# Kernel optimization log

Measured on AMD Instinct MI355X. Metric: run time of the kernel, lower is better.

## Reference

```python
import jax, jax.numpy as jnp
import numpy as np

B, S, D, H = 4, 2048, 1024, 16
DK = D // H
DFF = 4 * D
EPS = 1e-6


def setup_inputs() -> dict:
    key = jax.random.key(0)
    ks = jax.random.split(key, 16)
    s = 0.02
    return {
        "x": jax.random.normal(ks[0], (B, S, D), jnp.float32),
        "mask": jax.random.randint(ks[1], (B, 1, 1, S), 0, 2, jnp.int32),
        "wq": jax.random.normal(ks[2], (D, D), jnp.float32) * s,
        "bq": jnp.zeros((D,), jnp.float32),
        "wk": jax.random.normal(ks[3], (D, D), jnp.float32) * s,
        "bk": jnp.zeros((D,), jnp.float32),
        "wv": jax.random.normal(ks[4], (D, D), jnp.float32) * s,
        "bv": jnp.zeros((D,), jnp.float32),
        "wo": jax.random.normal(ks[5], (D, D), jnp.float32) * s,
        "bo": jnp.zeros((D,), jnp.float32),
        "w1": jax.random.normal(ks[6], (DFF, D), jnp.float32) * s,
        "b1": jnp.zeros((DFF,), jnp.float32),
        "w2": jax.random.normal(ks[7], (D, DFF), jnp.float32) * s,
        "b2": jnp.zeros((D,), jnp.float32),
        "a1": jnp.ones((1,), jnp.float32),
        "c1": jnp.zeros((1,), jnp.float32),
        "a2": jnp.ones((1,), jnp.float32),
        "c2": jnp.zeros((1,), jnp.float32),
    }


def _layernorm(x, alpha, bias):
    # source: alpha * (x - mean) / (std + eps) + bias, torch std is unbiased
    mean = jnp.mean(x, axis=-1, keepdims=True)
    std = jnp.std(x, axis=-1, keepdims=True, ddof=1)
    return alpha * (x - mean) / (std + EPS) + bias


def _mha(x, mask, wq, bq, wk, bk, wv, bv, wo, bo):
    q = (x @ wq.T + bq).reshape(B, S, H, DK).transpose(0, 2, 1, 3)  # [B,H,S,DK]
    k = (x @ wk.T + bk).reshape(B, S, H, DK).transpose(0, 2, 1, 3)
    v = (x @ wv.T + bv).reshape(B, S, H, DK).transpose(0, 2, 1, 3)
    scores = jnp.einsum("bhqd,bhkd->bhqk", q, k) / jnp.sqrt(jnp.float32(DK))
    scores = jnp.where(mask == 0, jnp.float32(-1e9), scores)
    attn = jax.nn.softmax(scores, axis=-1)
    out = jnp.einsum("bhqk,bhkd->bhqd", attn, v)  # [B,H,S,DK]
    out = out.transpose(0, 2, 1, 3).reshape(B, S, D)
    return out @ wo.T + bo


def reference(x, mask, wq, bq, wk, bk, wv, bv, wo, bo, w1, b1, w2, b2, a1, c1, a2, c2):
    # residual 1: x + MHA(LN(x))  (dropout = identity in eval)
    h = x + _mha(_layernorm(x, a1, c1), mask, wq, bq, wk, bk, wv, bv, wo, bo)
    # residual 2: h + FFN(LN(h))
    hn = _layernorm(h, a2, c2)
    ffn = jax.nn.relu(hn @ w1.T + b1) @ w2.T + b2
    return h + ffn
```

## Files before the change

### kernel.cpp

```cpp
#include <hip/hip_runtime.h>
#include <math.h>

static constexpr int B  = 4;
static constexpr int S  = 2048;
static constexpr int D  = 1024;
static constexpr int H  = 16;
static constexpr int DFF = 4096;

typedef __attribute__((ext_vector_type(8))) short short8;
typedef __attribute__((ext_vector_type(8))) unsigned short ushort8;
typedef __attribute__((ext_vector_type(4))) unsigned short ushort4v;
typedef __attribute__((ext_vector_type(4))) float f32x4;

__device__ __forceinline__ float b2f(unsigned short u) {
  unsigned int x = ((unsigned int)u) << 16;
  float f;
  __builtin_memcpy(&f, &x, 4);
  return f;
}
__device__ __forceinline__ unsigned short f2b(float f) {
  unsigned int x;
  __builtin_memcpy(&x, &f, 4);
  x += 0x7fffu + ((x >> 16) & 1u);
  return (unsigned short)(x >> 16);
}

__device__ __forceinline__ unsigned int cvtpk_bf16(float lo, float hi) {
  unsigned int r;
  asm("v_cvt_pk_bf16_f32 %0, %1, %2" : "=v"(r) : "v"(lo), "v"(hi));
  return r;
}

__device__ __forceinline__ f32x4 mfma16(short8 a, short8 b, f32x4 c) {
  return __builtin_amdgcn_mfma_f32_16x16x32_bf16(a, b, c, 0, 0, 0);
}

__device__ __forceinline__ void gload_lds16(const void* gsrc, void* ldst) {
  __builtin_amdgcn_global_load_lds(
      (__attribute__((address_space(1))) void*)(uintptr_t)gsrc,
      (__attribute__((address_space(3))) void*)ldst, 16, 0, 0);
}

#define VMC0 asm volatile("s_waitcnt vmcnt(0)" ::: "memory")
#define SB0  __builtin_amdgcn_sched_barrier(0)
#define BAR  __builtin_amdgcn_s_barrier()
#define PRIO1 __builtin_amdgcn_s_setprio(1)
#define PRIO0 __builtin_amdgcn_s_setprio(0)

struct CvtArgs {
  const float* s[6];
  unsigned short* d[6];
  int n[6];
};
__global__ __launch_bounds__(256) void convert6(CvtArgs a) {
  const int seg = blockIdx.y;
  const int i = (blockIdx.x * 256 + threadIdx.x) * 4;
  if (i < a.n[seg]) {
    f32x4 v = *(const f32x4*)(a.s[seg] + i);
    ushort4v o;
#pragma unroll
    for (int j = 0; j < 4; j++) o[j] = f2b(v[j]);
    *(ushort4v*)(a.d[seg] + i) = o;
  }
}

__global__ __launch_bounds__(256) void ln_fused(const float* __restrict__ x,
                                                const float* __restrict__ ap,
                                                const float* __restrict__ cp,
                                                unsigned short* __restrict__ out) {
  const int row = blockIdx.x, tid = threadIdx.x;
  const size_t base = (size_t)row * D;
  float v[4];
  float s = 0.f, sq = 0.f;
#pragma unroll
  for (int i = 0; i < 4; i++) {
    v[i] = x[base + tid + i * 256];
    s += v[i];
    sq += v[i] * v[i];
  }
#pragma unroll
  for (int o = 32; o > 0; o >>= 1) {
    s += __shfl_xor(s, o);
    sq += __shfl_xor(sq, o);
  }
  __shared__ __align__(16) float rs[4], rq[4];
  const int wave = tid >> 6, lane = tid & 63;
  if (lane == 0) {
    rs[wave] = s;
    rq[wave] = sq;
  }
  __syncthreads();
  const float S1 = rs[0] + rs[1] + rs[2] + rs[3];
  const float S2 = rq[0] + rq[1] + rq[2] + rq[3];
  const float mean = S1 * (1.f / 1024.f);
  const float var = fmaxf(0.f, (S2 - 1024.f * mean * mean) * (1.f / 1023.f));
  const float rstd = 1.f / (sqrtf(var) + 1e-6f);
  const float alpha = ap[0], beta = cp[0];
#pragma unroll
  for (int i = 0; i < 4; i++)
    out[base + tid + i * 256] = f2b(alpha * (v[i] - mean) * rstd + beta);
}

template <int EPI>
__global__ __launch_bounds__(256) void gemm_bb(
    const unsigned short* __restrict__ A, const unsigned short* __restrict__ W,
    const float* __restrict__ bias0, const float* __restrict__ bias1,
    const float* __restrict__ bias2, const float* __restrict__ resid,
    void* __restrict__ out, unsigned short* __restrict__ outK,
    unsigned short* __restrict__ outV, int M, int N, int K, int ldw) {
  __shared__ __align__(16) unsigned short As[128 * 32];
  __shared__ __align__(16) unsigned short Bs[128 * 32];
  const int tid = threadIdx.x;
  const int lane = tid & 63, wave = tid >> 6;
  const int quad = lane >> 4, l16 = lane & 15;
  const int m0 = blockIdx.y * 128, n0 = blockIdx.x * 128;
  const int wm = (wave >> 1) * 64, wn = (wave & 1) * 64;

  f32x4 acc[4][4];
#pragma unroll
  for (int i = 0; i < 4; i++)
#pragma unroll
    for (int j = 0; j < 4; j++) acc[i][j] = {0.f, 0.f, 0.f, 0.f};

  const int rA = tid >> 2;
  const int kc = (tid & 3) * 8;

  for (int k0 = 0; k0 < K; k0 += 32) {
    __syncthreads();
#pragma unroll
    for (int i = 0; i < 2; i++) {
      const int row = i * 64 + rA;
      gload_lds16(&A[(size_t)(m0 + row) * K + k0 + kc], &As[(i * 256 + wave * 64) * 8]);
      gload_lds16(&W[(size_t)(n0 + row) * ldw + k0 + kc], &Bs[(i * 256 + wave * 64) * 8]);
    }
    __syncthreads();
    short8 af[4], bf[4];
#pragma unroll
    for (int t = 0; t < 4; t++) {
      af[t] = *(const short8*)&As[(wm + t * 16 + l16) * 32 + quad * 8];
      bf[t] = *(const short8*)&Bs[(wn + t * 16 + l16) * 32 + quad * 8];
    }
#pragma unroll
    for (int mt = 0; mt < 4; mt++)
#pragma unroll
      for (int nt = 0; nt < 4; nt++) acc[mt][nt] = mfma16(af[mt], bf[nt], acc[mt][nt]);
  }

  if (EPI == 4) {
    const int band = (n0 + wn) >> 10;
    const float* bp = band == 0 ? bias0 : (band == 1 ? bias1 : bias2);
#pragma unroll
    for (int nt = 0; nt < 4; nt++) {
      const int col = n0 + wn + nt * 16 + l16;
      const int cl = col & 1023;
      const float bv = bp[cl];
#pragma unroll
      for (int mt = 0; mt < 4; mt++) {
#pragma unroll
        for (int r = 0; r < 4; r++) {
          const int row = m0 + wm + mt * 16 + quad * 4 + r;
          const float v = acc[mt][nt][r] + bv;
          if (band == 0)
            ((unsigned short*)out)[(size_t)row * 1024 + cl] = f2b(v);
          else if (band == 1)
            outK[(size_t)row * 1024 + cl] = f2b(v);
          else
            outV[((size_t)((row >> 11) * 1024 + cl)) * 2048 + (row & 2047)] = f2b(v);
        }
      }
    }
  } else {
#pragma unroll
    for (int nt = 0; nt < 4; nt++) {
      const int col = n0 + wn + nt * 16 + l16;
      const float bv = (EPI == 3) ? 0.f : bias0[col];
#pragma unroll
      for (int mt = 0; mt < 4; mt++) {
#pragma unroll
        for (int r = 0; r < 4; r++) {
          const int row = m0 + wm + mt * 16 + quad * 4 + r;
          const size_t idx = (size_t)row * N + col;
          float v = acc[mt][nt][r] + bv;
          if (EPI == 2) {
            v = fmaxf(v, 0.f);
            ((unsigned short*)out)[idx] = f2b(v);
          } else {
            v += resid[idx];
            ((float*)out)[idx] = v;
          }
        }
      }
    }
  }
}

__device__ __forceinline__ void attn_stage(const unsigned short* Kg,
                                           const unsigned short* Vg,
                                           unsigned short* Kd, unsigned short* Vd,
                                           int kt) {
  gload_lds16(Kg + (size_t)kt * 64 * D, Kd);
  gload_lds16(Kg + (size_t)kt * 64 * D + 8 * (size_t)D, Kd + 8 * 64);
  gload_lds16(Vg + (size_t)kt * 64, Vd);
  gload_lds16(Vg + (size_t)kt * 64 + 8 * (size_t)S, Vd + 8 * 64);
}

__global__ __launch_bounds__(256) void attn_kernel(unsigned short* __restrict__ Q,
                                                   const unsigned short* __restrict__ Kb,
                                                   const unsigned short* __restrict__ VT,
                                                   const int* __restrict__ mask) {
  __shared__ __align__(16) unsigned short Ks[64 * 64];
  __shared__ __align__(16) unsigned short Vs[64 * 64];
  constexpr int PPAD = 72;
  __shared__ __align__(16) unsigned short Pb[4][16 * PPAD];

  const int tid = threadIdx.x, lane = tid & 63, wave = tid >> 6;
  const int quad = lane >> 4, l16 = lane & 15;
  const int q0 = blockIdx.x * 64;
  const int b = blockIdx.y >> 4, h = blockIdx.y & 15;

  const int sr = lane >> 3;
  const int sc8 = ((lane & 7) ^ sr) * 8;
  const unsigned short* Kg = Kb + ((size_t)b * S + wave * 16 + sr) * D + h * 64 + sc8;
  const unsigned short* Vg = VT + ((size_t)blockIdx.y * 64 + wave * 16 + sr) * S + sc8;
  unsigned short* Kd = &Ks[(wave * 16) * 64];
  unsigned short* Vd = &Vs[(wave * 16) * 64];

  short8 qf0, qf1;
  {
    const int qr = q0 + wave * 16 + l16;
    const unsigned short* qp = &Q[((size_t)(b * S) + qr) * D + h * 64 + quad * 8];
    qf0 = *(const short8*)qp;
    qf1 = *(const short8*)(qp + 32);
  }

  float l_acc = 0.f;
  f32x4 o_acc[4];
#pragma unroll
  for (int t = 0; t < 4; t++) o_acc[t] = {0.f, 0.f, 0.f, 0.f};

  const int xr = l16 & 7;
  const int c0 = (quad ^ xr) * 8;
  const int c1 = ((quad + 4) ^ xr) * 8;

  for (int kt = 0; kt < S / 64; kt++) {
    const int k0 = kt * 64;
    BAR;
    attn_stage(Kg, Vg, Kd, Vd, kt);
    VMC0;
    SB0;
    BAR;

    f32x4 sc4[4];
#pragma unroll
    for (int nt = 0; nt < 4; nt++) sc4[nt] = {0.f, 0.f, 0.f, 0.f};
    PRIO1;
#pragma unroll
    for (int nt = 0; nt < 4; nt++) {
      short8 kf0 = *(const short8*)&Ks[(nt * 16 + l16) * 64 + c0];
      short8 kf1 = *(const short8*)&Ks[(nt * 16 + l16) * 64 + c1];
      sc4[nt] = mfma16(kf0, qf0, sc4[nt]);
      sc4[nt] = mfma16(kf1, qf1, sc4[nt]);
    }
    PRIO0;

#pragma unroll
    for (int nt = 0; nt < 4; nt++) {
      const int4 mv = *(const int4*)&mask[b * S + k0 + nt * 16 + quad * 4];
      const float p0 = __expf(fmaf(sc4[nt][0], 0.125f, mv.x ? -12.f : -42.f));
      const float p1 = __expf(fmaf(sc4[nt][1], 0.125f, mv.y ? -12.f : -42.f));
      const float p2 = __expf(fmaf(sc4[nt][2], 0.125f, mv.z ? -12.f : -42.f));
      const float p3 = __expf(fmaf(sc4[nt][3], 0.125f, mv.w ? -12.f : -42.f));
      l_acc += (p0 + p1) + (p2 + p3);
      uint2 pw;
      pw.x = cvtpk_bf16(p0, p1);
      pw.y = cvtpk_bf16(p2, p3);
      *(uint2*)&Pb[wave][l16 * PPAD + nt * 16 + quad * 4] = pw;
    }

    short8 pf0 = *(const short8*)&Pb[wave][l16 * PPAD + quad * 8];
    short8 pf1 = *(const short8*)&Pb[wave][l16 * PPAD + 32 + quad * 8];
    PRIO1;
#pragma unroll
    for (int nt = 0; nt < 4; nt++) {
      short8 vf0 = *(const short8*)&Vs[(nt * 16 + l16) * 64 + c0];
      short8 vf1 = *(const short8*)&Vs[(nt * 16 + l16) * 64 + c1];
      o_acc[nt] = mfma16(pf0, vf0, o_acc[nt]);
      o_acc[nt] = mfma16(pf1, vf1, o_acc[nt]);
    }
    PRIO0;
  }

  l_acc += __shfl_xor(l_acc, 16);
  l_acc += __shfl_xor(l_acc, 32);

#pragma unroll
  for (int r = 0; r < 4; r++) {
    const float lr = __shfl(l_acc, quad * 4 + r);
    const float inv = 1.f / lr;
    const int q = q0 + wave * 16 + quad * 4 + r;
#pragma unroll
    for (int nt = 0; nt < 4; nt++) {
      const int dk = nt * 16 + l16;
      Q[((size_t)(b * S) + q) * D + h * 64 + dk] = f2b(o_acc[nt][r] * inv);
    }
  }
}

__global__ __launch_bounds__(256) void stats_kernel(const float* __restrict__ x,
                                                    float2* __restrict__ st) {
  const int row = blockIdx.x, tid = threadIdx.x;
  const size_t base = (size_t)row * D;
  float s = 0.f, sq = 0.f;
#pragma unroll
  for (int i = 0; i < 4; i++) {
    const float v = x[base + tid + i * 256];
    s += v;
    sq += v * v;
  }
#pragma unroll
  for (int o = 32; o > 0; o >>= 1) {
    s += __shfl_xor(s, o);
    sq += __shfl_xor(sq, o);
  }
  __shared__ __align__(16) float rs[4], rq[4];
  const int wave = tid >> 6, lane = tid & 63;
  if (lane == 0) {
    rs[wave] = s;
    rq[wave] = sq;
  }
  __syncthreads();
  if (tid == 0) {
    const float S1 = rs[0] + rs[1] + rs[2] + rs[3];
    const float S2 = rq[0] + rq[1] + rq[2] + rq[3];
    const float mean = S1 * (1.f / 1024.f);
    const float var = fmaxf(0.f, (S2 - 1024.f * mean * mean) * (1.f / 1023.f));
    const float rstd = 1.f / (sqrtf(var) + 1e-6f);
    st[row] = make_float2(mean, rstd);
  }
}

template <int EPI, int NORM, int AF32, int OUTF32>
__global__ __launch_bounds__(256) void gemm_bt(
    const void* __restrict__ Ap, const float* __restrict__ W,
    const float* __restrict__ bias, const float* __restrict__ resid,
    void* __restrict__ outp, const float2* __restrict__ stats,
    const float* __restrict__ alpha_p, const float* __restrict__ beta_p,
    int M, int N, int K, int ldw) {
  __shared__ __align__(16) unsigned short As[128 * 32];
  __shared__ __align__(16) unsigned short Bs[128 * 32];
  const int tid = threadIdx.x;
  const int lane = tid & 63, wave = tid >> 6;
  const int quad = lane >> 4, l16 = lane & 15;
  const int m0 = blockIdx.y * 128, n0 = blockIdx.x * 128;
  const int wm = (wave >> 1) * 64, wn = (wave & 1) * 64;

  float alpha = 0.f, beta = 0.f;
  if (NORM) {
    alpha = alpha_p[0];
    beta = beta_p[0];
  }

  f32x4 acc[4][4];
#pragma unroll
  for (int i = 0; i < 4; i++)
#pragma unroll
    for (int j = 0; j < 4; j++) acc[i][j] = {0.f, 0.f, 0.f, 0.f};

  const int rA = tid >> 2;
  const int kc = (tid & 3) * 8;

  for (int k0 = 0; k0 < K; k0 += 32) {
    ushort8 av[2], bv8[2];
#pragma unroll
    for (int i = 0; i < 2; i++) {
      const int row = i * 64 + rA;
      if (AF32) {
        const float* ap = (const float*)Ap + (size_t)(m0 + row) * K + k0 + kc;
        f32x4 a0 = *(const f32x4*)ap;
        f32x4 a1 = *(const f32x4*)(ap + 4);
        if (NORM) {
          const float2 st = stats[m0 + row];
#pragma unroll
          for (int j = 0; j < 4; j++) {
            a0[j] = alpha * (a0[j] - st.x) * st.y + beta;
            a1[j] = alpha * (a1[j] - st.x) * st.y + beta;
          }
        }
#pragma unroll
        for (int j = 0; j < 4; j++) {
          av[i][j] = f2b(a0[j]);
          av[i][j + 4] = f2b(a1[j]);
        }
      } else {
        av[i] = *(const ushort8*)((const unsigned short*)Ap +
                                  (size_t)(m0 + row) * K + k0 + kc);
      }
      const float* wp = W + (size_t)(n0 + row) * ldw + k0 + kc;
      f32x4 w0 = *(const f32x4*)wp;
      f32x4 w1 = *(const f32x4*)(wp + 4);
#pragma unroll
      for (int j = 0; j < 4; j++) {
        bv8[i][j] = f2b(w0[j]);
        bv8[i][j + 4] = f2b(w1[j]);
      }
    }
    __syncthreads();
#pragma unroll
    for (int i = 0; i < 2; i++) {
      const int row = i * 64 + rA;
      *(ushort8*)&As[row * 32 + kc] = av[i];
      *(ushort8*)&Bs[row * 32 + kc] = bv8[i];
    }
    __syncthreads();
    short8 af[4], bf[4];
#pragma unroll
    for (int t = 0; t < 4; t++) {
      af[t] = *(const short8*)&As[(wm + t * 16 + l16) * 32 + quad * 8];
      bf[t] = *(const short8*)&Bs[(wn + t * 16 + l16) * 32 + quad * 8];
    }
#pragma unroll
    for (int mt = 0; mt < 4; mt++)
#pragma unroll
      for (int nt = 0; nt < 4; nt++) acc[mt][nt] = mfma16(af[mt], bf[nt], acc[mt][nt]);
  }

#pragma unroll
  for (int nt = 0; nt < 4; nt++) {
    const int col = n0 + wn + nt * 16 + l16;
    const float bv = (EPI == 3) ? 0.f : bias[col];
#pragma unroll
    for (int mt = 0; mt < 4; mt++) {
#pragma unroll
      for (int r = 0; r < 4; r++) {
        const int row = m0 + wm + mt * 16 + quad * 4 + r;
        float v = acc[mt][nt][r] + bv;
        if (EPI == 2) v = fmaxf(v, 0.f);
        if (EPI == 4) {
          const size_t vtidx =
              ((size_t)((row >> 11) * 1024 + col)) * 2048 + (row & 2047);
          ((unsigned short*)outp)[vtidx] = f2b(v);
        } else {
          const size_t idx = (size_t)row * N + col;
          if (EPI == 1 || EPI == 3) v += resid[idx];
          if (OUTF32)
            ((float*)outp)[idx] = v;
          else
            ((unsigned short*)outp)[idx] = f2b(v);
        }
      }
    }
  }
}

extern "C" void kernel_launch(void* const* d_in, const int* in_sizes, int n_in,
                              void* d_out, int out_size, void* d_ws, size_t ws_size,
                              hipStream_t stream) {
  (void)in_sizes; (void)n_in; (void)out_size;
  const float* x  = (const float*)d_in[0];
  const int* mask = (const int*)d_in[1];
  const float* wq = (const float*)d_in[2];
  const float* bq = (const float*)d_in[3];
  const float* wk = (const float*)d_in[4];
  const float* bk = (const float*)d_in[5];
  const float* wv = (const float*)d_in[6];
  const float* bv = (const float*)d_in[7];
  const float* wo = (const float*)d_in[8];
  const float* bo = (const float*)d_in[9];
  const float* w1 = (const float*)d_in[10];
  const float* b1 = (const float*)d_in[11];
  const float* w2 = (const float*)d_in[12];
  const float* b2 = (const float*)d_in[13];
  const float* a1 = (const float*)d_in[14];
  const float* c1 = (const float*)d_in[15];
  const float* a2 = (const float*)d_in[16];
  const float* c2 = (const float*)d_in[17];

  char* ws = (char*)d_ws;
  const size_t MB = 1 << 20;
  const int M = B * S;
  dim3 blk(256);
  dim3 gAttn(S / 64, B * H);

  if (ws_size >= 89 * MB) {
    const int tier3 = (ws_size >= 152 * MB);
    const int tier2 = (ws_size >= 121 * MB);
    unsigned short* wqkv_b = (unsigned short*)(ws + 0);
    unsigned short* wo_b   = (unsigned short*)(ws + 6 * MB);
    unsigned short* w1_b   = (unsigned short*)(ws + 8 * MB);
    unsigned short* w2_b   = (unsigned short*)(ws + 16 * MB);
    unsigned short* ln1x   = (unsigned short*)(ws + 25 * MB);
    unsigned short* q      = (unsigned short*)(ws + 41 * MB);
    unsigned short* kk     = (unsigned short*)(ws + 57 * MB);
    unsigned short* vt     = (unsigned short*)(ws + 73 * MB);
    float*          hbuf   = (float*)(ws + 57 * MB);
    unsigned short* ln2x   = (unsigned short*)(ws + 25 * MB);
    unsigned short* ffn1q  = (unsigned short*)(ws + 41 * MB);
    unsigned short* ffn1h  = (unsigned short*)(ws + 89 * MB);
    unsigned short* ffn1f  = (unsigned short*)(ws + 89 * MB);
    float* outb = (float*)d_out;

    CvtArgs ca;
    ca.s[0] = wq; ca.d[0] = wqkv_b;            ca.n[0] = 1048576;
    ca.s[1] = wk; ca.d[1] = wqkv_b + 1048576;  ca.n[1] = 1048576;
    ca.s[2] = wv; ca.d[2] = wqkv_b + 2097152;  ca.n[2] = 1048576;
    ca.s[3] = wo; ca.d[3] = wo_b;              ca.n[3] = 1048576;
    ca.s[4] = w1; ca.d[4] = w1_b;              ca.n[4] = 4194304;
    ca.s[5] = w2; ca.d[5] = w2_b;              ca.n[5] = 4194304;
    convert6<<<dim3(4096, 6), blk, 0, stream>>>(ca);

    ln_fused<<<M, blk, 0, stream>>>(x, a1, c1, ln1x);
    gemm_bb<4><<<dim3(24, 64), blk, 0, stream>>>(ln1x, wqkv_b, bq, bk, bv, nullptr,
                                                 q, kk, vt, M, 3072, D, D);
    attn_kernel<<<gAttn, blk, 0, stream>>>(q, kk, vt, mask);
    gemm_bb<1><<<dim3(8, 64), blk, 0, stream>>>(q, wo_b, bo, nullptr, nullptr, x,
                                                hbuf, nullptr, nullptr, M, D, D, D);
    ln_fused<<<M, blk, 0, stream>>>(hbuf, a2, c2, ln2x);

    if (tier3) {
      gemm_bb<2><<<dim3(32, 64), blk, 0, stream>>>(ln2x, w1_b, b1, nullptr, nullptr,
                                                   nullptr, ffn1f, nullptr, nullptr,
                                                   M, DFF, D, D);
      gemm_bb<1><<<dim3(8, 64), blk, 0, stream>>>(ffn1f, w2_b, b2, nullptr, nullptr,
                                                  hbuf, outb, nullptr, nullptr,
                                                  M, D, DFF, DFF);
    } else if (tier2) {
      gemm_bb<2><<<dim3(16, 64), blk, 0, stream>>>(ln2x, w1_b, b1, nullptr, nullptr,
                                                   nullptr, ffn1h, nullptr, nullptr,
                                                   M, 2048, D, D);
      gemm_bb<1><<<dim3(8, 64), blk, 0, stream>>>(ffn1h, w2_b, b2, nullptr, nullptr,
                                                  hbuf, outb, nullptr, nullptr,
                                                  M, D, 2048, DFF);
      gemm_bb<2><<<dim3(16, 64), blk, 0, stream>>>(ln2x, w1_b + (size_t)2048 * D,
                                                   b1 + 2048, nullptr, nullptr, nullptr,
                                                   ffn1h, nullptr, nullptr, M, 2048, D, D);
      gemm_bb<3><<<dim3(8, 64), blk, 0, stream>>>(ffn1h, w2_b + 2048, nullptr, nullptr,
                                                  nullptr, outb, outb, nullptr, nullptr,
                                                  M, D, 2048, DFF);
    } else {
      for (int i = 0; i < 4; i++) {
        gemm_bb<2><<<dim3(8, 64), blk, 0, stream>>>(ln2x, w1_b + (size_t)i * 1024 * D,
                                                    b1 + i * 1024, nullptr, nullptr,
                                                    nullptr, ffn1q, nullptr, nullptr,
                                                    M, 1024, D, D);
        if (i == 0)
          gemm_bb<1><<<dim3(8, 64), blk, 0, stream>>>(ffn1q, w2_b + i * 1024, b2, nullptr,
                                                      nullptr, hbuf, outb, nullptr, nullptr,
                                                      M, D, 1024, DFF);
        else
          gemm_bb<3><<<dim3(8, 64), blk, 0, stream>>>(ffn1q, w2_b + i * 1024, nullptr,
                                                      nullptr, nullptr, outb, outb, nullptr,
                                                      nullptr, M, D, 1024, DFF);
      }
    }
  } else {
    float2* stats1 = (float2*)(ws + 0);
    float2* stats2 = (float2*)(ws + 128 * 1024);
    unsigned short* q    = (unsigned short*)(ws + 1 * MB);
    unsigned short* kk   = (unsigned short*)(ws + 17 * MB);
    unsigned short* vt   = (unsigned short*)(ws + 33 * MB);
    float*          hbuf = (float*)(ws + 17 * MB);
    unsigned short* ffn1 = (unsigned short*)(ws + 1 * MB);
    float* outb = (float*)d_out;
    dim3 gD(D / 128, M / 128);

    stats_kernel<<<M, blk, 0, stream>>>(x, stats1);
    gemm_bt<0, 1, 1, 0><<<gD, blk, 0, stream>>>(x, wq, bq, nullptr, q, stats1, a1, c1, M, D, D, D);
    gemm_bt<0, 1, 1, 0><<<gD, blk, 0, stream>>>(x, wk, bk, nullptr, kk, stats1, a1, c1, M, D, D, D);
    gemm_bt<4, 1, 1, 0><<<gD, blk, 0, stream>>>(x, wv, bv, nullptr, vt, stats1, a1, c1, M, D, D, D);
    attn_kernel<<<gAttn, blk, 0, stream>>>(q, kk, vt, mask);
    gemm_bt<1, 0, 0, 1><<<gD, blk, 0, stream>>>(q, wo, bo, x, hbuf, nullptr, nullptr, nullptr, M, D, D, D);
    stats_kernel<<<M, blk, 0, stream>>>(hbuf, stats2);
    for (int i = 0; i < 4; i++) {
      gemm_bt<2, 1, 1, 0><<<gD, blk, 0, stream>>>(hbuf, w1 + (size_t)i * 1024 * D,
                                                  b1 + i * 1024, nullptr, ffn1, stats2,
                                                  a2, c2, M, 1024, D, D);
      if (i == 0)
        gemm_bt<1, 0, 0, 1><<<gD, blk, 0, stream>>>(ffn1, w2 + i * 1024, b2, hbuf, outb,
                                                    nullptr, nullptr, nullptr, M, D, 1024, DFF);
      else
        gemm_bt<3, 0, 0, 1><<<gD, blk, 0, stream>>>(ffn1, w2 + i * 1024, nullptr, outb, outb,
                                                    nullptr, nullptr, nullptr, M, D, 1024, DFF);
    }
  }
}
```

Before: 605.9 us.

## Process 128 queries per attention block, two 16-row query tiles per wave

Each wave of the attention kernel now handles two 16-row query tiles, so a block covers 128 queries and the grid halves. Every K/V tile staged in LDS is reused across twice as many query rows, halving global K/V traffic and barrier rounds per unit of work. In exchange each wave holds twice the accumulators, score fragments and Q fragments, which raises register pressure and the P scratch buffer size. Launch bounds are also changed to request four blocks per multiprocessor.

```diff
diff --git a/kernel.cpp b/kernel.cpp
--- a/kernel.cpp
+++ b/kernel.cpp
@@ -204,18 +204,18 @@
   gload_lds16(Vg + (size_t)kt * 64 + 8 * (size_t)S, Vd + 8 * 64);
 }
 
-__global__ __launch_bounds__(256) void attn_kernel(unsigned short* __restrict__ Q,
-                                                   const unsigned short* __restrict__ Kb,
-                                                   const unsigned short* __restrict__ VT,
-                                                   const int* __restrict__ mask) {
+__global__ __launch_bounds__(256, 4) void attn_kernel(unsigned short* __restrict__ Q,
+                                                      const unsigned short* __restrict__ Kb,
+                                                      const unsigned short* __restrict__ VT,
+                                                      const int* __restrict__ mask) {
   __shared__ __align__(16) unsigned short Ks[64 * 64];
   __shared__ __align__(16) unsigned short Vs[64 * 64];
   constexpr int PPAD = 72;
-  __shared__ __align__(16) unsigned short Pb[4][16 * PPAD];
+  __shared__ __align__(16) unsigned short Pb[8][16 * PPAD];
 
   const int tid = threadIdx.x, lane = tid & 63, wave = tid >> 6;
   const int quad = lane >> 4, l16 = lane & 15;
-  const int q0 = blockIdx.x * 64;
+  const int q0 = blockIdx.x * 128;
   const int b = blockIdx.y >> 4, h = blockIdx.y & 15;
 
   const int sr = lane >> 3;
@@ -225,18 +225,21 @@
   unsigned short* Kd = &Ks[(wave * 16) * 64];
   unsigned short* Vd = &Vs[(wave * 16) * 64];
 
-  short8 qf0, qf1;
-  {
-    const int qr = q0 + wave * 16 + l16;
-    const unsigned short* qp = &Q[((size_t)(b * S) + qr) * D + h * 64 + quad * 8];
-    qf0 = *(const short8*)qp;
-    qf1 = *(const short8*)(qp + 32);
-  }
-
-  float l_acc = 0.f;
-  f32x4 o_acc[4];
-#pragma unroll
-  for (int t = 0; t < 4; t++) o_acc[t] = {0.f, 0.f, 0.f, 0.f};
+  short8 qf[2][2];
+#pragma unroll
+  for (int qh = 0; qh < 2; qh++) {
+    const unsigned short* qp =
+        &Q[((size_t)b * S + q0 + wave * 32 + qh * 16 + l16) * D + h * 64 + quad * 8];
+    qf[qh][0] = *(const short8*)qp;
+    qf[qh][1] = *(const short8*)(qp + 32);
+  }
+
+  float l_acc[2] = {0.f, 0.f};
+  f32x4 o_acc[2][4];
+#pragma unroll
+  for (int qh = 0; qh < 2; qh++)
+#pragma unroll
+    for (int t = 0; t < 4; t++) o_acc[qh][t] = {0.f, 0.f, 0.f, 0.f};
 
   const int xr = l16 & 7;
   const int c0 = (quad ^ xr) * 8;
@@ -250,58 +253,78 @@
     SB0;
     BAR;
 
-    f32x4 sc4[4];
-#pragma unroll
-    for (int nt = 0; nt < 4; nt++) sc4[nt] = {0.f, 0.f, 0.f, 0.f};
+    f32x4 sc4[2][4];
+#pragma unroll
+    for (int qh = 0; qh < 2; qh++)
+#pragma unroll
+      for (int nt = 0; nt < 4; nt++) sc4[qh][nt] = {0.f, 0.f, 0.f, 0.f};
     PRIO1;
 #pragma unroll
     for (int nt = 0; nt < 4; nt++) {
       short8 kf0 = *(const short8*)&Ks[(nt * 16 + l16) * 64 + c0];
       short8 kf1 = *(const short8*)&Ks[(nt * 16 + l16) * 64 + c1];
-      sc4[nt] = mfma16(kf0, qf0, sc4[nt]);
-      sc4[nt] = mfma16(kf1, qf1, sc4[nt]);
+      sc4[0][nt] = mfma16(kf0, qf[0][0], sc4[0][nt]);
+      sc4[0][nt] = mfma16(kf1, qf[0][1], sc4[0][nt]);
+      sc4[1][nt] = mfma16(kf0, qf[1][0], sc4[1][nt]);
+      sc4[1][nt] = mfma16(kf1, qf[1][1], sc4[1][nt]);
     }
     PRIO0;
 
 #pragma unroll
     for (int nt = 0; nt < 4; nt++) {
       const int4 mv = *(const int4*)&mask[b * S + k0 + nt * 16 + quad * 4];
-      const float p0 = __expf(fmaf(sc4[nt][0], 0.125f, mv.x ? -12.f : -42.f));
-      const float p1 = __expf(fmaf(sc4[nt][1], 0.125f, mv.y ? -12.f : -42.f));
-      const float p2 = __expf(fmaf(sc4[nt][2], 0.125f, mv.z ? -12.f : -42.f));
-      const float p3 = __expf(fmaf(sc4[nt][3], 0.125f, mv.w ? -12.f : -42.f));
-      l_acc += (p0 + p1) + (p2 + p3);
-      uint2 pw;
-      pw.x = cvtpk_bf16(p0, p1);
-      pw.y = cvtpk_bf16(p2, p3);
-      *(uint2*)&Pb[wave][l16 * PPAD + nt * 16 + quad * 4] = pw;
-    }
-
-    short8 pf0 = *(const short8*)&Pb[wave][l16 * PPAD + quad * 8];
-    short8 pf1 = *(const short8*)&Pb[wave][l16 * PPAD + 32 + quad * 8];
+      const float m0f = mv.x ? -12.f : -42.f;
+      const float m1f = mv.y ? -12.f : -42.f;
+      const float m2f = mv.z ? -12.f : -42.f;
+      const float m3f = mv.w ? -12.f : -42.f;
+#pragma unroll
+      for (int qh = 0; qh < 2; qh++) {
+        const float p0 = __expf(fmaf(sc4[qh][nt][0], 0.125f, m0f));
+        const float p1 = __expf(fmaf(sc4[qh][nt][1], 0.125f, m1f));
+        const float p2 = __expf(fmaf(sc4[qh][nt][2], 0.125f, m2f));
+        const float p3 = __expf(fmaf(sc4[qh][nt][3], 0.125f, m3f));
+        l_acc[qh] += (p0 + p1) + (p2 + p3);
+        uint2 pw;
+        pw.x = cvtpk_bf16(p0, p1);
+        pw.y = cvtpk_bf16(p2, p3);
+        *(uint2*)&Pb[wave * 2 + qh][l16 * PPAD + nt * 16 + quad * 4] = pw;
+      }
+    }
+
+    short8 pf[2][2];
+#pragma unroll
+    for (int qh = 0; qh < 2; qh++) {
+      pf[qh][0] = *(const short8*)&Pb[wave * 2 + qh][l16 * PPAD + quad * 8];
+      pf[qh][1] = *(const short8*)&Pb[wave * 2 + qh][l16 * PPAD + 32 + quad * 8];
+    }
     PRIO1;
 #pragma unroll
     for (int nt = 0; nt < 4; nt++) {
       short8 vf0 = *(const short8*)&Vs[(nt * 16 + l16) * 64 + c0];
       short8 vf1 = *(const short8*)&Vs[(nt * 16 + l16) * 64 + c1];
-      o_acc[nt] = mfma16(pf0, vf0, o_acc[nt]);
-      o_acc[nt] = mfma16(pf1, vf1, o_acc[nt]);
+      o_acc[0][nt] = mfma16(pf[0][0], vf0, o_acc[0][nt]);
+      o_acc[0][nt] = mfma16(pf[0][1], vf1, o_acc[0][nt]);
+      o_acc[1][nt] = mfma16(pf[1][0], vf0, o_acc[1][nt]);
+      o_acc[1][nt] = mfma16(pf[1][1], vf1, o_acc[1][nt]);
     }
     PRIO0;
   }
 
-  l_acc += __shfl_xor(l_acc, 16);
-  l_acc += __shfl_xor(l_acc, 32);
-
-#pragma unroll
-  for (int r = 0; r < 4; r++) {
-    const float lr = __shfl(l_acc, quad * 4 + r);
-    const float inv = 1.f / lr;
-    const int q = q0 + wave * 16 + quad * 4 + r;
-#pragma unroll
-    for (int nt = 0; nt < 4; nt++) {
-      const int dk = nt * 16 + l16;
-      Q[((size_t)(b * S) + q) * D + h * 64 + dk] = f2b(o_acc[nt][r] * inv);
+#pragma unroll
+  for (int qh = 0; qh < 2; qh++) {
+    float la = l_acc[qh];
+    la += __shfl_xor(la, 16);
+    la += __shfl_xor(la, 32);
+#pragma unroll
+    for (int r = 0; r < 4; r++) {
+      const float lr = __shfl(la, quad * 4 + r);
+      const float inv = 1.f / lr;
+      const int q = q0 + wave * 32 + qh * 16 + quad * 4 + r;
+#pragma unroll
+      for (int nt = 0; nt < 4; nt++) {
+        const int dk = nt * 16 + l16;
+        Q[((size_t)b * S + q) * D + h * 64 + dk] = f2b(o_acc[qh][nt][r] * inv);
+      }
     }
   }
 }
@@ -479,7 +502,7 @@
   const size_t MB = 1 << 20;
   const int M = B * S;
   dim3 blk(256);
-  dim3 gAttn(S / 64, B * H);
+  dim3 gAttn(S / 128, B * H);
 
   if (ws_size >= 89 * MB) {
     const int tier3 = (ws_size >= 152 * MB);
```

Result: no change. 596.0 us (-1.6%).
